# Performance work log

Measured on AMD Instinct MI355X. Metric: run time of the kernel, lower is better.

Reference implementation:

```python
import jax, jax.numpy as jnp
import numpy as np

V, BLOCK, L, H, C = 50257, 1024, 4, 12, 768
HS = C // H  # 64
EPS = 1e-6  # flax LayerNorm default


def _ln(x, scale, bias):
    mu = jnp.mean(x, axis=-1, keepdims=True)
    var = jnp.var(x, axis=-1, keepdims=True)
    return (x - mu) * jax.lax.rsqrt(var + EPS) * scale + bias


def setup_inputs() -> dict:
    key = jax.random.key(0)
    ks = jax.random.split(key, 12)
    B, T = 2, 1024
    inp = {
        'idx': jax.random.randint(ks[0], (B, T), 0, V),
        'targets': jax.random.randint(ks[1], (B, T), 0, V),
        'wte': jax.random.normal(ks[2], (V, C), jnp.float32) * 0.02,
        'wpe': jax.random.normal(ks[3], (BLOCK, C), jnp.float32) * 0.02,
        'ln1_s': jnp.ones((L, C), jnp.float32),
        'ln1_b': jnp.zeros((L, C), jnp.float32),
        'attn_k': jax.random.normal(ks[4], (L, C, H, 3 * HS), jnp.float32) * 0.02,
        'attn_b': jnp.zeros((L, H, 3 * HS), jnp.float32),
        'aproj_k': jax.random.normal(ks[5], (L, C, C), jnp.float32) * 0.02,
        'aproj_b': jnp.zeros((L, C), jnp.float32),
        'ln2_s': jnp.ones((L, C), jnp.float32),
        'ln2_b': jnp.zeros((L, C), jnp.float32),
        'fc_k': jax.random.normal(ks[6], (L, C, 4 * C), jnp.float32) * 0.02,
        'fc_b': jnp.zeros((L, 4 * C), jnp.float32),
        'mproj_k': jax.random.normal(ks[7], (L, 4 * C, C), jnp.float32) * 0.02,
        'mproj_b': jnp.zeros((L, C), jnp.float32),
        'lnf_s': jnp.ones((C,), jnp.float32),
        'lnf_b': jnp.zeros((C,), jnp.float32),
    }
    return inp


def _block(x, ln1_s, ln1_b, Wqkv, bqkv, Wo, bo, ln2_s, ln2_b, Wfc, bfc, Wmp, bmp, mask):
    B, T, _ = x.shape
    h = _ln(x, ln1_s, ln1_b)
    qkv = jnp.einsum('btc,chd->bhtd', h, Wqkv) + bqkv[:, None, :]  # [B,H,T,3HS]
    q, k, v = jnp.split(qkv, 3, axis=-1)
    att = jnp.einsum('bhtd,bhsd->bhts', q, k) * (1.0 / jnp.sqrt(jnp.float32(HS)))
    att = jnp.where(mask, att, -jnp.inf)
    att = jax.nn.softmax(att, axis=-1)
    y = jnp.einsum('bhts,bhsd->bthd', att, v).reshape(B, T, C)
    x = x + y @ Wo + bo
    h = _ln(x, ln2_s, ln2_b)
    h = jax.nn.gelu(h @ Wfc + bfc, approximate=True)
    x = x + h @ Wmp + bmp
    return x


def reference(idx, targets, wte, wpe, ln1_s, ln1_b, attn_k, attn_b, aproj_k, aproj_b,
              ln2_s, ln2_b, fc_k, fc_b, mproj_k, mproj_b, lnf_s, lnf_b):
    B, T = idx.shape
    x = wte[idx] + wpe[jnp.arange(T)][None]  # [B,T,C]
    mask = jnp.tril(jnp.ones((T, T), bool))[None, None]
    for l in range(L):
        x = _block(x, ln1_s[l], ln1_b[l], attn_k[l], attn_b[l], aproj_k[l], aproj_b[l],
                   ln2_s[l], ln2_b[l], fc_k[l], fc_b[l], mproj_k[l], mproj_b[l], mask)
    x = _ln(x, lnf_s, lnf_b)
    logits = jnp.einsum('btc,vc->btv', x, wte)  # tied output projection (wte.attend)
    logp = jax.nn.log_softmax(logits, axis=-1)
    loss = -jnp.mean(jnp.take_along_axis(logp, targets[..., None], axis=-1))
    return logits, loss
```

## Files before the change

### kernel.cpp

```cpp
#include <hip/hip_runtime.h>
#include <hip/hip_bf16.h>
#include <math.h>

typedef __attribute__((ext_vector_type(8))) short bf16x8;
typedef __attribute__((ext_vector_type(4))) float f32x4;

static constexpr int Bv   = 2;
static constexpr int Tv   = 1024;
static constexpr int Cv   = 768;
static constexpr int Hv   = 12;
static constexpr int Lv   = 4;
static constexpr int Vv   = 50257;
static constexpr int Mv   = 2048;
static constexpr int NTv  = 393;
static constexpr float EPSv = 1e-6f;

__device__ __forceinline__ void gload16(const void* g, void* l) {
    __builtin_amdgcn_global_load_lds((const __attribute__((address_space(1))) void*)g,
                                     (__attribute__((address_space(3))) void*)l, 16, 0, 0);
}
template<int N>
__device__ __forceinline__ void waitvm_barrier() {
    if constexpr (N == 0)      asm volatile("s_waitcnt vmcnt(0)\ns_barrier" ::: "memory");
    else if constexpr (N == 2) asm volatile("s_waitcnt vmcnt(2)\ns_barrier" ::: "memory");
    else if constexpr (N == 3) asm volatile("s_waitcnt vmcnt(3)\ns_barrier" ::: "memory");
    else if constexpr (N == 4) asm volatile("s_waitcnt vmcnt(4)\ns_barrier" ::: "memory");
    else if constexpr (N == 6) asm volatile("s_waitcnt vmcnt(6)\ns_barrier" ::: "memory");
    else                       asm volatile("s_waitcnt vmcnt(8)\ns_barrier" ::: "memory");
}
__device__ __forceinline__ void lgkm0_barrier() {
    asm volatile("s_waitcnt lgkmcnt(0)\ns_barrier" ::: "memory");
}

__global__ void embed_kernel(const int* __restrict__ idx,
                             const float* __restrict__ wte,
                             const float* __restrict__ wpe,
                             float* __restrict__ x) {
    int row = blockIdx.x;
    int t   = row & (Tv - 1);
    int tok = idx[row];
    const float* src = wte + (size_t)tok * Cv;
    const float* pos = wpe + (size_t)t * Cv;
    float* dst = x + (size_t)row * Cv;
    for (int c = threadIdx.x; c < Cv; c += 256)
        dst[c] = src[c] + pos[c];
}

__device__ __forceinline__ ushort4 pack4bf(float4 v) {
    ushort4 u;
    u.x = __bfloat16_as_ushort(__float2bfloat16(v.x));
    u.y = __bfloat16_as_ushort(__float2bfloat16(v.y));
    u.z = __bfloat16_as_ushort(__float2bfloat16(v.z));
    u.w = __bfloat16_as_ushort(__float2bfloat16(v.w));
    return u;
}

__global__ void ln_kernel(const float* __restrict__ in,
                          const float* __restrict__ sc,
                          const float* __restrict__ bi,
                          __hip_bfloat16* __restrict__ out) {
    int row  = blockIdx.x * 4 + (threadIdx.x >> 6);
    int lane = threadIdx.x & 63;
    const float4* xr = (const float4*)(in + (size_t)row * Cv);
    float4 a = xr[lane], b = xr[lane + 64], c = xr[lane + 128];
    float sum = a.x + a.y + a.z + a.w + b.x + b.y + b.z + b.w + c.x + c.y + c.z + c.w;
    float sq  = a.x*a.x + a.y*a.y + a.z*a.z + a.w*a.w
              + b.x*b.x + b.y*b.y + b.z*b.z + b.w*b.w
              + c.x*c.x + c.y*c.y + c.z*c.z + c.w*c.w;
    #pragma unroll
    for (int off = 32; off; off >>= 1) {
        sum += __shfl_xor(sum, off, 64);
        sq  += __shfl_xor(sq,  off, 64);
    }
    float mean = sum * (1.0f / Cv);
    float var  = sq * (1.0f / Cv) - mean * mean;
    float rs   = rsqrtf(var + EPSv);
    const float4* s4 = (const float4*)sc;
    const float4* b4 = (const float4*)bi;
    ushort4* orow = (ushort4*)(out + (size_t)row * Cv);
    #pragma unroll
    for (int i = 0; i < 3; ++i) {
        float4 v = (i == 0) ? a : (i == 1) ? b : c;
        float4 s = s4[lane + 64 * i];
        float4 t = b4[lane + 64 * i];
        float4 o;
        o.x = (v.x - mean) * rs * s.x + t.x;
        o.y = (v.y - mean) * rs * s.y + t.y;
        o.z = (v.z - mean) * rs * s.z + t.z;
        o.w = (v.w - mean) * rs * s.w + t.w;
        orow[lane + 64 * i] = pack4bf(o);
    }
}

__global__ void wtrans_kernel(const float* __restrict__ in,
                              __hip_bfloat16* __restrict__ out, int K, int N) {
    __shared__ float tile[32][33];
    int k0 = blockIdx.y * 32, n0 = blockIdx.x * 32;
    int tx = threadIdx.x & 31, ty = threadIdx.x >> 5;
    #pragma unroll
    for (int i = 0; i < 4; ++i)
        tile[ty + i * 8][tx] = in[(size_t)(k0 + ty + i * 8) * N + n0 + tx];
    __syncthreads();
    #pragma unroll
    for (int i = 0; i < 4; ++i)
        out[(size_t)(n0 + ty + i * 8) * K + k0 + tx] =
            __float2bfloat16(tile[tx][ty + i * 8]);
}

__global__ void cvt_kernel(const float* __restrict__ in,
                           __hip_bfloat16* __restrict__ out, int n4) {
    int stride = gridDim.x * 256;
    for (int i = blockIdx.x * 256 + threadIdx.x; i < n4; i += stride) {
        float4 v = ((const float4*)in)[i];
        ((ushort4*)out)[i] = pack4bf(v);
    }
}

__global__ void vtrans_kernel(const __hip_bfloat16* __restrict__ qkv,
                              __hip_bfloat16* __restrict__ vt) {
    __shared__ __hip_bfloat16 tile[32][33];
    int bh = blockIdx.z;
    int b = bh / Hv, h = bh % Hv;
    int t0 = blockIdx.x * 32, d0 = blockIdx.y * 32;
    int tx = threadIdx.x & 31, ty = threadIdx.x >> 5;
    #pragma unroll
    for (int i = 0; i < 4; ++i)
        tile[ty + i * 8][tx] =
            qkv[(size_t)(b * Tv + t0 + ty + i * 8) * 2304 + h * 192 + 128 + d0 + tx];
    __syncthreads();
    #pragma unroll
    for (int i = 0; i < 4; ++i)
        vt[((size_t)bh * 64 + d0 + ty + i * 8) * Tv + t0 + tx] = tile[tx][ty + i * 8];
}

template<int EPI, int BM>
__launch_bounds__(256)
__global__ void gemm_bf16(const __hip_bfloat16* __restrict__ A,
                          const __hip_bfloat16* __restrict__ Bt,
                          const float* __restrict__ bias,
                          const float* R, float* Cf,
                          __hip_bfloat16* __restrict__ Cb,
                          int M, int N, int K) {
    constexpr int FM  = BM / 32;
    constexpr int NA  = BM / 64;
    constexpr int LPT = NA + 1;
    __shared__ __hip_bfloat16 As[3][BM * 32];
    __shared__ __hip_bfloat16 Bs[3][64 * 32];
    int tid = threadIdx.x;
    int wave = tid >> 6, lane = tid & 63;
    int wr = wave >> 1, wc = wave & 1;
    int rowBase = blockIdx.y * BM, colBase = blockIdx.x * 64;

    f32x4 acc[FM][2] = {};

    int srow  = wave * 16 + (lane >> 2);
    int skcol = (lane & 3) * 8;
    const __hip_bfloat16* Ap0 = A + (size_t)(rowBase + srow) * K + skcol;
    const __hip_bfloat16* Ap1 = (NA > 1) ? (Ap0 + (size_t)64 * K) : Ap0;
    const __hip_bfloat16* Bp0 = Bt + (size_t)(colBase + srow) * K + skcol;
    int ldso = wave * 512;

    int aoff = (wr * (BM / 2) + (lane & 15)) * 32 + (lane >> 4) * 8;
    int boff = (wc * 32 + (lane & 15)) * 32 + (lane >> 4) * 8;

    auto stage = [&](int buf) {
        gload16(Ap0, &As[buf][ldso]);
        if constexpr (NA > 1) gload16(Ap1, &As[buf][2048 + ldso]);
        gload16(Bp0, &Bs[buf][ldso]);
        Ap0 += 32;
        if constexpr (NA > 1) Ap1 += 32;
        Bp0 += 32;
    };

    stage(0); stage(1); stage(2);

    int nt = K / 32;
    int cur = 0;
    for (int t = 0; t < nt; ++t) {
        if (t < nt - 2)       waitvm_barrier<2 * LPT>();
        else if (t == nt - 2) waitvm_barrier<LPT>();
        else                  waitvm_barrier<0>();

        bf16x8 av[FM], bv[2];
        #pragma unroll
        for (int m = 0; m < FM; ++m) av[m] = *(const bf16x8*)&As[cur][aoff + m * 512];
        #pragma unroll
        for (int n = 0; n < 2; ++n)  bv[n] = *(const bf16x8*)&Bs[cur][boff + n * 512];
        lgkm0_barrier();

        if (t + 3 < nt) stage(cur);

        #pragma unroll
        for (int m = 0; m < FM; ++m)
            #pragma unroll
            for (int n = 0; n < 2; ++n)
                acc[m][n] = __builtin_amdgcn_mfma_f32_16x16x32_bf16(
                    av[m], bv[n], acc[m][n], 0, 0, 0);
        cur = (cur == 2) ? 0 : cur + 1;
    }

    int fq = lane >> 4, fr = lane & 15;
    #pragma unroll
    for (int m = 0; m < FM; ++m) {
        #pragma unroll
        for (int n = 0; n < 2; ++n) {
            f32x4 v = acc[m][n];
            int col = colBase + wc * 32 + n * 16 + fr;
            #pragma unroll
            for (int j = 0; j < 4; ++j) {
                int row = rowBase + wr * (BM / 2) + m * 16 + fq * 4 + j;
                float val = v[j] + bias[col];
                if (EPI == 1) {
                    val += R[(size_t)row * N + col];
                    Cf[(size_t)row * N + col] = val;
                } else {
                    if (EPI == 2) {
                        float u = val;
                        float cc = 0.7978845608028654f * (u + 0.044715f * u * u * u);
                        val = 0.5f * u * (1.0f + tanhf(cc));
                    }
                    Cb[(size_t)row * N + col] = __float2bfloat16(val);
                }
            }
        }
    }
}

__launch_bounds__(256)
__global__ void attn_kernel(const __hip_bfloat16* __restrict__ qkv,
                            const __hip_bfloat16* __restrict__ vt,
                            __hip_bfloat16* __restrict__ att) {
    __shared__ __hip_bfloat16 Qs[64 * 64];
    __shared__ __hip_bfloat16 Ks[64 * 64];
    __shared__ __hip_bfloat16 Vs[64 * 64];
    __shared__ __hip_bfloat16 Ps[64 * 64];
    int bh = blockIdx.x;
    int b = bh / Hv, h = bh % Hv;
    int qt = (int)gridDim.y - 1 - (int)blockIdx.y;
    int q0 = qt * 64;
    int tid = threadIdx.x, wave = tid >> 6, lane = tid & 63;
    int g = lane >> 4, fr = lane & 15;
    int srow8 = lane >> 3, sc8 = lane & 7;

    const __hip_bfloat16* qbase = qkv + (size_t)(b * Tv + q0) * 2304 + h * 192;
    #pragma unroll
    for (int i = 0; i < 2; ++i) {
        int row = wave * 16 + i * 8 + srow8;
        gload16(qbase + (size_t)row * 2304 + ((sc8 ^ (row & 7)) * 8),
                Qs + (wave * 16 + i * 8) * 64);
    }

    f32x4 accO[4] = {};
    float mrun[4] = {-1e30f, -1e30f, -1e30f, -1e30f};
    float lrun[4] = {0.f, 0.f, 0.f, 0.f};

    for (int kv = 0; kv <= qt; ++kv) {
        int s0 = kv * 64;
        __syncthreads();
        const __hip_bfloat16* kbase = qkv + (size_t)(b * Tv + s0) * 2304 + h * 192 + 64;
        const __hip_bfloat16* vbase = vt + (size_t)bh * 64 * Tv + s0;
        #pragma unroll
        for (int i = 0; i < 2; ++i) {
            int row = wave * 16 + i * 8 + srow8;
            gload16(kbase + (size_t)row * 2304 + ((sc8 ^ (row & 7)) * 8),
                    Ks + (wave * 16 + i * 8) * 64);
            gload16(vbase + (size_t)row * Tv + ((sc8 ^ (row & 7)) * 8),
                    Vs + (wave * 16 + i * 8) * 64);
        }
        __syncthreads();

        f32x4 s4[4] = {};
        #pragma unroll
        for (int kk = 0; kk < 2; ++kk) {
            int qrow = wave * 16 + fr;
            bf16x8 qa = *(const bf16x8*)&Qs[qrow * 64 + (((g + 4 * kk) ^ (fr & 7)) * 8)];
            #pragma unroll
            for (int n = 0; n < 4; ++n) {
                int krow = n * 16 + fr;
                bf16x8 kb = *(const bf16x8*)&Ks[krow * 64 + (((g + 4 * kk) ^ (fr & 7)) * 8)];
                s4[n] = __builtin_amdgcn_mfma_f32_16x16x32_bf16(qa, kb, s4[n], 0, 0, 0);
            }
        }

        bool dia = (kv == qt);
        #pragma unroll
        for (int j = 0; j < 4; ++j) {
            int qg = q0 + wave * 16 + g * 4 + j;
            float sj[4], mx = -1e30f;
            #pragma unroll
            for (int n = 0; n < 4; ++n) {
                float v = s4[n][j] * 0.125f;
                if (dia && (s0 + n * 16 + fr) > qg) v = -1e30f;
                sj[n] = v;
                mx = fmaxf(mx, v);
            }
            #pragma unroll
            for (int off = 1; off < 16; off <<= 1)
                mx = fmaxf(mx, __shfl_xor(mx, off, 64));
            float mnew = fmaxf(mrun[j], mx);
            float ps = 0.f;
            unsigned short pb[4];
            #pragma unroll
            for (int n = 0; n < 4; ++n) {
                float p = __expf(sj[n] - mnew);
                __hip_bfloat16 pc = __float2bfloat16(p);
                pb[n] = __bfloat16_as_ushort(pc);
                ps += __bfloat162float(pc);
            }
            #pragma unroll
            for (int off = 1; off < 16; off <<= 1)
                ps += __shfl_xor(ps, off, 64);
            float cr = __expf(mrun[j] - mnew);
            lrun[j] = lrun[j] * cr + ps;
            mrun[j] = mnew;
            int prow = wave * 16 + g * 4 + j;
            #pragma unroll
            for (int n = 0; n < 4; ++n) {
                int byteoff = (32 * n + 2 * fr) ^ ((prow & 7) << 4);
                ((unsigned short*)Ps)[prow * 64 + (byteoff >> 1)] = pb[n];
            }
            #pragma unroll
            for (int n = 0; n < 4; ++n) accO[n][j] *= cr;
        }
        __syncthreads();

        #pragma unroll
        for (int kk = 0; kk < 2; ++kk) {
            int prow = wave * 16 + fr;
            bf16x8 pa = *(const bf16x8*)&Ps[prow * 64 + (((g + 4 * kk) ^ (fr & 7)) * 8)];
            #pragma unroll
            for (int n = 0; n < 4; ++n) {
                int vrow = n * 16 + fr;
                bf16x8 vb = *(const bf16x8*)&Vs[vrow * 64 + (((g + 4 * kk) ^ (fr & 7)) * 8)];
                accO[n] = __builtin_amdgcn_mfma_f32_16x16x32_bf16(pa, vb, accO[n], 0, 0, 0);
            }
        }
    }

    #pragma unroll
    for (int j = 0; j < 4; ++j) {
        float inv = 1.0f / lrun[j];
        int row = b * Tv + q0 + wave * 16 + g * 4 + j;
        #pragma unroll
        for (int n = 0; n < 4; ++n)
            att[(size_t)row * Cv + h * 64 + n * 16 + fr] =
                __float2bfloat16(accO[n][j] * inv);
    }
}

__launch_bounds__(256)
__global__ void lmhead_kernel(const __hip_bfloat16* __restrict__ A,
                              const __hip_bfloat16* __restrict__ Bt,
                              float* __restrict__ Cf,
                              float* __restrict__ pLse) {
    constexpr int K = Cv, N = Vv;
    __shared__ __hip_bfloat16 As[3][4096];
    __shared__ __hip_bfloat16 Bs[3][4096];
    __shared__ float ps2[2][128];

    int bid = blockIdx.x;
    int nid = (bid & 7) * (NTv * 16 / 8) + (bid >> 3);
    int rowT = nid & 15, colT = nid >> 4;
    int rowBase = rowT * 128, colBase = colT * 128;

    int tid = threadIdx.x, wave = tid >> 6, lane = tid & 63;
    int wr = wave >> 1, wc = wave & 1;

    f32x4 acc[4][4] = {};

    int srow  = wave * 16 + (lane >> 2);
    int skcol = (lane & 3) * 8;
    const __hip_bfloat16* Ap  = A + (size_t)(rowBase + srow) * K + skcol;
    const __hip_bfloat16* Ap2 = Ap + (size_t)64 * K;
    int brow1 = colBase + srow;
    int brow2 = brow1 + 64;
    const __hip_bfloat16* Bp  = Bt + (size_t)brow1 * K + skcol;
    const __hip_bfloat16* Bp2 = Bt + (size_t)(brow2 < N ? brow2 : N - 1) * K + skcol;
    int ldso = wave * 512;

    int aoff = (wr * 64 + (lane & 15)) * 32 + (lane >> 4) * 8;
    int boff = (wc * 64 + (lane & 15)) * 32 + (lane >> 4) * 8;

    auto stage = [&](int buf) {
        gload16(Ap,  &As[buf][ldso]);
        gload16(Ap2, &As[buf][2048 + ldso]);
        gload16(Bp,  &Bs[buf][ldso]);
        gload16(Bp2, &Bs[buf][2048 + ldso]);
        Ap += 32; Ap2 += 32; Bp += 32; Bp2 += 32;
    };

    stage(0); stage(1); stage(2);

    constexpr int nt = K / 32;
    int cur = 0;
    for (int t = 0; t < nt; ++t) {
        if (t < nt - 2)       waitvm_barrier<8>();
        else if (t == nt - 2) waitvm_barrier<4>();
        else                  waitvm_barrier<0>();

        bf16x8 av[4], bv[4];
        #pragma unroll
        for (int m = 0; m < 4; ++m) av[m] = *(const bf16x8*)&As[cur][aoff + m * 512];
        #pragma unroll
        for (int n = 0; n < 4; ++n) bv[n] = *(const bf16x8*)&Bs[cur][boff + n * 512];
        lgkm0_barrier();

        if (t + 3 < nt) stage(cur);

        #pragma unroll
        for (int m = 0; m < 4; ++m)
            #pragma unroll
            for (int n = 0; n < 4; ++n)
                acc[m][n] = __builtin_amdgcn_mfma_f32_16x16x32_bf16(
                    av[m], bv[n], acc[m][n], 0, 0, 0);
        cur = (cur == 2) ? 0 : cur + 1;
    }

    int fq = lane >> 4, fr = lane & 15;

    #pragma unroll
    for (int m = 0; m < 4; ++m) {
        #pragma unroll
        for (int j = 0; j < 4; ++j) {
            int row = rowBase + wr * 64 + m * 16 + fq * 4 + j;
            float s = 0.f;
            #pragma unroll
            for (int n = 0; n < 4; ++n) {
                int col = colBase + wc * 64 + n * 16 + fr;
                float v = acc[m][n][j];
                if (col < N) {
                    Cf[(size_t)row * N + col] = v;
                    s += __expf(v);
                }
            }
            #pragma unroll
            for (int off = 1; off < 16; off <<= 1)
                s += __shfl_xor(s, off, 64);
            if (fr == 0)
                ps2[wc][wr * 64 + m * 16 + fq * 4 + j] = s;
        }
    }
    __syncthreads();
    if (tid < 128)
        pLse[(size_t)(rowBase + tid) * NTv + colT] = ps2[0][tid] + ps2[1][tid];
}

__global__ void plse_reduce_kernel(const float* __restrict__ pLse,
                                   const float* __restrict__ logits,
                                   const int* __restrict__ targets,
                                   float* __restrict__ rloss) {
    int row  = blockIdx.x * 4 + (threadIdx.x >> 6);
    int lane = threadIdx.x & 63;
    const float* pr = pLse + (size_t)row * NTv;
    float l = 0.f;
    for (int i = lane; i < NTv; i += 64) l += pr[i];
    #pragma unroll
    for (int off = 32; off; off >>= 1) l += __shfl_xor(l, off, 64);
    if (lane == 0)
        rloss[row] = logf(l) - logits[(size_t)row * Vv + targets[row]];
}

__global__ void loss_final_kernel(const float* __restrict__ rloss,
                                  float* __restrict__ out, int out_size) {
    float s = 0.f;
    for (int i = threadIdx.x; i < Mv; i += 256) s += rloss[i];
    #pragma unroll
    for (int off = 32; off; off >>= 1) s += __shfl_xor(s, off, 64);
    __shared__ float sw[4];
    int wave = threadIdx.x >> 6, lane = threadIdx.x & 63;
    if (lane == 0) sw[wave] = s;
    __syncthreads();
    if (threadIdx.x == 0)
        out[out_size - 1] = (sw[0] + sw[1] + sw[2] + sw[3]) / (float)Mv;
}

extern "C" void kernel_launch(void* const* d_in, const int* in_sizes, int n_in,
                              void* d_out, int out_size, void* d_ws, size_t ws_size,
                              hipStream_t stream) {
    const int*   idx     = (const int*)  d_in[0];
    const int*   targets = (const int*)  d_in[1];
    const float* wte     = (const float*)d_in[2];
    const float* wpe     = (const float*)d_in[3];
    const float* ln1_s   = (const float*)d_in[4];
    const float* ln1_b   = (const float*)d_in[5];
    const float* attn_k  = (const float*)d_in[6];
    const float* attn_b  = (const float*)d_in[7];
    const float* aproj_k = (const float*)d_in[8];
    const float* aproj_b = (const float*)d_in[9];
    const float* ln2_s   = (const float*)d_in[10];
    const float* ln2_b   = (const float*)d_in[11];
    const float* fc_k    = (const float*)d_in[12];
    const float* fc_b    = (const float*)d_in[13];
    const float* mproj_k = (const float*)d_in[14];
    const float* mproj_b = (const float*)d_in[15];
    const float* lnf_s   = (const float*)d_in[16];
    const float* lnf_b   = (const float*)d_in[17];

    float* out = (float*)d_out;
    char* ws  = (char*)d_ws;
    char* ob  = (char*)d_out;

    constexpr size_t NEED = 83568128ULL;
    if (ws_size < NEED) return;

    __hip_bfloat16* wte_bf = (__hip_bfloat16*)(ws + 0);
    __hip_bfloat16* h_bf   = (__hip_bfloat16*)(ws + 77194752);
    float*          pLse   = (float*)(ws + 80340480);
    float*          rloss  = (float*)(ws + 83559936);

    float*          x      = (float*)(ob + 0);
    __hip_bfloat16* qkv_bf = (__hip_bfloat16*)(ob + 6291456);
    __hip_bfloat16* vt_bf  = (__hip_bfloat16*)(ob + 15728640);
    __hip_bfloat16* att_bf = (__hip_bfloat16*)(ob + 18874368);
    __hip_bfloat16* fco_bf = (__hip_bfloat16*)(ob + 22020096);
    __hip_bfloat16* w0     = (__hip_bfloat16*)(ob + 34603008);
    __hip_bfloat16* w1     = (__hip_bfloat16*)(ob + 38141952);
    __hip_bfloat16* w2     = (__hip_bfloat16*)(ob + 39321600);
    __hip_bfloat16* w3     = (__hip_bfloat16*)(ob + 44040192);

    embed_kernel<<<Mv, 256, 0, stream>>>(idx, wte, wpe, x);

    for (int l = 0; l < Lv; ++l) {
        wtrans_kernel<<<dim3(72, 24), 256, 0, stream>>>(
            attn_k + (size_t)l * Cv * 2304, w0, Cv, 2304);
        wtrans_kernel<<<dim3(24, 24), 256, 0, stream>>>(
            aproj_k + (size_t)l * Cv * Cv, w1, Cv, Cv);
        wtrans_kernel<<<dim3(96, 24), 256, 0, stream>>>(
            fc_k + (size_t)l * Cv * 3072, w2, Cv, 3072);
        wtrans_kernel<<<dim3(24, 96), 256, 0, stream>>>(
            mproj_k + (size_t)l * 3072 * Cv, w3, 3072, Cv);

        ln_kernel<<<512, 256, 0, stream>>>(x, ln1_s + l * Cv, ln1_b + l * Cv, h_bf);
        gemm_bf16<0, 128><<<dim3(36, 16), 256, 0, stream>>>(
            h_bf, w0, attn_b + l * 2304, nullptr, nullptr, qkv_bf, Mv, 2304, Cv);
        vtrans_kernel<<<dim3(32, 2, 24), 256, 0, stream>>>(qkv_bf, vt_bf);
        attn_kernel<<<dim3(24, 16), 256, 0, stream>>>(qkv_bf, vt_bf, att_bf);
        gemm_bf16<1, 64><<<dim3(12, 32), 256, 0, stream>>>(
            att_bf, w1, aproj_b + l * Cv, x, x, nullptr, Mv, Cv, Cv);
        ln_kernel<<<512, 256, 0, stream>>>(x, ln2_s + l * Cv, ln2_b + l * Cv, h_bf);
        gemm_bf16<2, 128><<<dim3(48, 16), 256, 0, stream>>>(
            h_bf, w2, fc_b + l * 3072, nullptr, nullptr, fco_bf, Mv, 3072, Cv);
        gemm_bf16<1, 64><<<dim3(12, 32), 256, 0, stream>>>(
            fco_bf, w3, mproj_b + l * Cv, x, x, nullptr, Mv, Cv, 3072);
    }

    ln_kernel<<<512, 256, 0, stream>>>(x, lnf_s, lnf_b, h_bf);
    cvt_kernel<<<2048, 256, 0, stream>>>(wte, wte_bf, (Vv * Cv) / 4);
    lmhead_kernel<<<16 * NTv, 256, 0, stream>>>(h_bf, wte_bf, out, pLse);
    plse_reduce_kernel<<<512, 256, 0, stream>>>(pLse, out, targets, rloss);
    loss_final_kernel<<<1, 256, 0, stream>>>(rloss, out, out_size);
}
```

Before: 986.8 us.

## Enlarge LM-head tiles to 256x256 with swizzled LDS and batch weight transposes

The LM-head GEMM now uses 256x256 output tiles with 512 threads, a 64-wide K step with double buffering, and an XOR-swizzled LDS layout. Wave priority is raised around the MFMA bursts. This cuts global/L2 traffic per FLOP and halves the partial-LSE columns. The per-layer weight transposes are collapsed into four launches that cover all layers, storing each layer's transposed weights separately. The larger tile means higher register pressure, only one block per CU, and more waste in the last partial vocabulary tile.

```diff
diff --git a/kernel.cpp b/kernel.cpp
--- a/kernel.cpp
+++ b/kernel.cpp
@@ -12,7 +12,7 @@
 static constexpr int Lv   = 4;
 static constexpr int Vv   = 50257;
 static constexpr int Mv   = 2048;
-static constexpr int NTv  = 393;
+static constexpr int NT2  = 197;
 static constexpr float EPSv = 1e-6f;
 
 __device__ __forceinline__ void gload16(const void* g, void* l) {
@@ -93,8 +93,11 @@
 }
 
 __global__ void wtrans_kernel(const float* __restrict__ in,
-                              __hip_bfloat16* __restrict__ out, int K, int N) {
+                              __hip_bfloat16* __restrict__ out, int K, int N,
+                              size_t inLS, size_t outLS) {
     __shared__ float tile[32][33];
+    in  += (size_t)blockIdx.z * inLS;
+    out += (size_t)blockIdx.z * outLS;
     int k0 = blockIdx.y * 32, n0 = blockIdx.x * 32;
     int tx = threadIdx.x & 31, ty = threadIdx.x >> 5;
     #pragma unroll
@@ -348,81 +351,107 @@
     }
 }
 
-__launch_bounds__(256)
+__launch_bounds__(512, 1)
 __global__ void lmhead_kernel(const __hip_bfloat16* __restrict__ A,
                               const __hip_bfloat16* __restrict__ Bt,
                               float* __restrict__ Cf,
                               float* __restrict__ pLse) {
     constexpr int K = Cv, N = Vv;
-    __shared__ __hip_bfloat16 As[3][4096];
-    __shared__ __hip_bfloat16 Bs[3][4096];
-    __shared__ float ps2[2][128];
+    constexpr int nt = K / 64;
+    __shared__ __hip_bfloat16 As[2][16384];
+    __shared__ __hip_bfloat16 Bs[2][16384];
+    __shared__ float ps[4][256];
 
     int bid = blockIdx.x;
-    int nid = (bid & 7) * (NTv * 16 / 8) + (bid >> 3);
-    int rowT = nid & 15, colT = nid >> 4;
-    int rowBase = rowT * 128, colBase = colT * 128;
-
-    int tid = threadIdx.x, wave = tid >> 6, lane = tid & 63;
-    int wr = wave >> 1, wc = wave & 1;
-
-    f32x4 acc[4][4] = {};
-
-    int srow  = wave * 16 + (lane >> 2);
-    int skcol = (lane & 3) * 8;
-    const __hip_bfloat16* Ap  = A + (size_t)(rowBase + srow) * K + skcol;
-    const __hip_bfloat16* Ap2 = Ap + (size_t)64 * K;
-    int brow1 = colBase + srow;
-    int brow2 = brow1 + 64;
-    const __hip_bfloat16* Bp  = Bt + (size_t)brow1 * K + skcol;
-    const __hip_bfloat16* Bp2 = Bt + (size_t)(brow2 < N ? brow2 : N - 1) * K + skcol;
-    int ldso = wave * 512;
-
-    int aoff = (wr * 64 + (lane & 15)) * 32 + (lane >> 4) * 8;
-    int boff = (wc * 64 + (lane & 15)) * 32 + (lane >> 4) * 8;
-
-    auto stage = [&](int buf) {
-        gload16(Ap,  &As[buf][ldso]);
-        gload16(Ap2, &As[buf][2048 + ldso]);
-        gload16(Bp,  &Bs[buf][ldso]);
-        gload16(Bp2, &Bs[buf][2048 + ldso]);
-        Ap += 32; Ap2 += 32; Bp += 32; Bp2 += 32;
+    int nid = (bid & 7) * NT2 + (bid >> 3);
+    int rowT = nid & 7, colT = nid >> 3;
+    int rowBase = rowT * 256, colBase = colT * 256;
+
+    int tid = threadIdx.x;
+    int wv = tid >> 6, lane = tid & 63;
+    int wr = wv >> 2, wc = wv & 3;
+    int fq = lane >> 4, fr = lane & 15;
+    int fr7 = fr & 7;
+
+    f32x4 acc[8][4] = {};
+
+    int r8 = lane >> 3;
+    int cOff = ((lane & 7) ^ r8) * 8;
+    const __hip_bfloat16* ApS[4];
+    const __hip_bfloat16* BpS[4];
+    #pragma unroll
+    for (int i = 0; i < 4; ++i) {
+        int rit = wv * 32 + i * 8 + r8;
+        ApS[i] = A + (size_t)(rowBase + rit) * K + cOff;
+        int rb = colBase + rit;
+        if (rb >= N) rb = N - 1;
+        BpS[i] = Bt + (size_t)rb * K + cOff;
+    }
+
+    auto stage = [&](int buf, int tile) {
+        int k0 = tile * 64;
+        #pragma unroll
+        for (int i = 0; i < 4; ++i)
+            gload16(ApS[i] + k0, &As[buf][(wv * 4 + i) * 512]);
+        #pragma unroll
+        for (int i = 0; i < 4; ++i)
+            gload16(BpS[i] + k0, &Bs[buf][(wv * 4 + i) * 512]);
     };
 
-    stage(0); stage(1); stage(2);
-
-    constexpr int nt = K / 32;
-    int cur = 0;
+    stage(0, 0);
+    stage(1, 1);
+    waitvm_barrier<8>();
+
     for (int t = 0; t < nt; ++t) {
-        if (t < nt - 2)       waitvm_barrier<8>();
-        else if (t == nt - 2) waitvm_barrier<4>();
-        else                  waitvm_barrier<0>();
-
-        bf16x8 av[4], bv[4];
-        #pragma unroll
-        for (int m = 0; m < 4; ++m) av[m] = *(const bf16x8*)&As[cur][aoff + m * 512];
-        #pragma unroll
-        for (int n = 0; n < 4; ++n) bv[n] = *(const bf16x8*)&Bs[cur][boff + n * 512];
-        lgkm0_barrier();
-
-        if (t + 3 < nt) stage(cur);
-
-        #pragma unroll
-        for (int m = 0; m < 4; ++m)
+        int cur = t & 1;
+        const __hip_bfloat16* Ab = &As[cur][0];
+        const __hip_bfloat16* Bb = &Bs[cur][0];
+
+        bf16x8 av0[8], bv0[4];
+        #pragma unroll
+        for (int m = 0; m < 8; ++m)
+            av0[m] = *(const bf16x8*)&Ab[(wr * 128 + m * 16 + fr) * 64 + ((fq ^ fr7) * 8)];
+        #pragma unroll
+        for (int n = 0; n < 4; ++n)
+            bv0[n] = *(const bf16x8*)&Bb[(wc * 64 + n * 16 + fr) * 64 + ((fq ^ fr7) * 8)];
+        __builtin_amdgcn_s_setprio(1);
+        #pragma unroll
+        for (int m = 0; m < 8; ++m)
             #pragma unroll
             for (int n = 0; n < 4; ++n)
                 acc[m][n] = __builtin_amdgcn_mfma_f32_16x16x32_bf16(
-                    av[m], bv[n], acc[m][n], 0, 0, 0);
-        cur = (cur == 2) ? 0 : cur + 1;
-    }
-
-    int fq = lane >> 4, fr = lane & 15;
-
-    #pragma unroll
-    for (int m = 0; m < 4; ++m) {
+                    av0[m], bv0[n], acc[m][n], 0, 0, 0);
+        __builtin_amdgcn_s_setprio(0);
+
+        bf16x8 av1[8], bv1[4];
+        #pragma unroll
+        for (int m = 0; m < 8; ++m)
+            av1[m] = *(const bf16x8*)&Ab[(wr * 128 + m * 16 + fr) * 64 + (((4 + fq) ^ fr7) * 8)];
+        #pragma unroll
+        for (int n = 0; n < 4; ++n)
+            bv1[n] = *(const bf16x8*)&Bb[(wc * 64 + n * 16 + fr) * 64 + (((4 + fq) ^ fr7) * 8)];
+        lgkm0_barrier();
+
+        if (t + 2 < nt) stage(cur, t + 2);
+
+        __builtin_amdgcn_s_setprio(1);
+        #pragma unroll
+        for (int m = 0; m < 8; ++m)
+            #pragma unroll
+            for (int n = 0; n < 4; ++n)
+                acc[m][n] = __builtin_amdgcn_mfma_f32_16x16x32_bf16(
+                    av1[m], bv1[n], acc[m][n], 0, 0, 0);
+        __builtin_amdgcn_s_setprio(0);
+
+        if (t + 2 < nt) waitvm_barrier<8>();
+        else            waitvm_barrier<0>();
+    }
+
+    #pragma unroll
+    for (int m = 0; m < 8; ++m) {
         #pragma unroll
         for (int j = 0; j < 4; ++j) {
-            int row = rowBase + wr * 64 + m * 16 + fq * 4 + j;
+            int row = rowBase + wr * 128 + m * 16 + fq * 4 + j;
             float s = 0.f;
             #pragma unroll
             for (int n = 0; n < 4; ++n) {
@@ -437,12 +466,13 @@
             for (int off = 1; off < 16; off <<= 1)
                 s += __shfl_xor(s, off, 64);
             if (fr == 0)
-                ps2[wc][wr * 64 + m * 16 + fq * 4 + j] = s;
+                ps[wc][wr * 128 + m * 16 + fq * 4 + j] = s;
         }
     }
     __syncthreads();
-    if (tid < 128)
-        pLse[(size_t)(rowBase + tid) * NTv + colT] = ps2[0][tid] + ps2[1][tid];
+    if (tid < 256)
+        pLse[(size_t)(rowBase + tid) * NT2 + colT] =
+            ps[0][tid] + ps[1][tid] + ps[2][tid] + ps[3][tid];
 }
 
 __global__ void plse_reduce_kernel(const float* __restrict__ pLse,
@@ -451,9 +481,9 @@
                                    float* __restrict__ rloss) {
     int row  = blockIdx.x * 4 + (threadIdx.x >> 6);
     int lane = threadIdx.x & 63;
-    const float* pr = pLse + (size_t)row * NTv;
+    const float* pr = pLse + (size_t)row * NT2;
     float l = 0.f;
-    for (int i = lane; i < NTv; i += 64) l += pr[i];
+    for (int i = lane; i < NT2; i += 64) l += pr[i];
     #pragma unroll
     for (int off = 32; off; off >>= 1) l += __shfl_xor(l, off, 64);
     if (lane == 0)
@@ -500,13 +530,13 @@
     char* ws  = (char*)d_ws;
     char* ob  = (char*)d_out;
 
-    constexpr size_t NEED = 83568128ULL;
+    constexpr size_t NEED = 81962496ULL;
     if (ws_size < NEED) return;
 
     __hip_bfloat16* wte_bf = (__hip_bfloat16*)(ws + 0);
     __hip_bfloat16* h_bf   = (__hip_bfloat16*)(ws + 77194752);
     float*          pLse   = (float*)(ws + 80340480);
-    float*          rloss  = (float*)(ws + 83559936);
+    float*          rloss  = (float*)(ws + 81954304);
 
     float*          x      = (float*)(ob + 0);
     __hip_bfloat16* qkv_bf = (__hip_bfloat16*)(ob + 6291456);
@@ -514,39 +544,43 @@
     __hip_bfloat16* att_bf = (__hip_bfloat16*)(ob + 18874368);
     __hip_bfloat16* fco_bf = (__hip_bfloat16*)(ob + 22020096);
     __hip_bfloat16* w0     = (__hip_bfloat16*)(ob + 34603008);
-    __hip_bfloat16* w1     = (__hip_bfloat16*)(ob + 38141952);
-    __hip_bfloat16* w2     = (__hip_bfloat16*)(ob + 39321600);
-    __hip_bfloat16* w3     = (__hip_bfloat16*)(ob + 44040192);
+    __hip_bfloat16* w1     = (__hip_bfloat16*)(ob + 48758784);
+    __hip_bfloat16* w2     = (__hip_bfloat16*)(ob + 53477376);
+    __hip_bfloat16* w3     = (__hip_bfloat16*)(ob + 72351744);
 
     embed_kernel<<<Mv, 256, 0, stream>>>(idx, wte, wpe, x);
 
+    wtrans_kernel<<<dim3(72, 24, 4), 256, 0, stream>>>(
+        attn_k, w0, Cv, 2304, (size_t)Cv * 2304, (size_t)2304 * Cv);
+    wtrans_kernel<<<dim3(24, 24, 4), 256, 0, stream>>>(
+        aproj_k, w1, Cv, Cv, (size_t)Cv * Cv, (size_t)Cv * Cv);
+    wtrans_kernel<<<dim3(96, 24, 4), 256, 0, stream>>>(
+        fc_k, w2, Cv, 3072, (size_t)Cv * 3072, (size_t)3072 * Cv);
+    wtrans_kernel<<<dim3(24, 96, 4), 256, 0, stream>>>(
+        mproj_k, w3, 3072, Cv, (size_t)3072 * Cv, (size_t)Cv * 3072);
+
     for (int l = 0; l < Lv; ++l) {
-        wtrans_kernel<<<dim3(72, 24), 256, 0, stream>>>(
-            attn_k + (size_t)l * Cv * 2304, w0, Cv, 2304);
-        wtrans_kernel<<<dim3(24, 24), 256, 0, stream>>>(
-            aproj_k + (size_t)l * Cv * Cv, w1, Cv, Cv);
-        wtrans_kernel<<<dim3(96, 24), 256, 0, stream>>>(
-            fc_k + (size_t)l * Cv * 3072, w2, Cv, 3072);
-        wtrans_kernel<<<dim3(24, 96), 256, 0, stream>>>(
-            mproj_k + (size_t)l * 3072 * Cv, w3, 3072, Cv);
-
         ln_kernel<<<512, 256, 0, stream>>>(x, ln1_s + l * Cv, ln1_b + l * Cv, h_bf);
         gemm_bf16<0, 128><<<dim3(36, 16), 256, 0, stream>>>(
-            h_bf, w0, attn_b + l * 2304, nullptr, nullptr, qkv_bf, Mv, 2304, Cv);
+            h_bf, w0 + (size_t)l * 2304 * Cv, attn_b + l * 2304, nullptr, nullptr,
+            qkv_bf, Mv, 2304, Cv);
         vtrans_kernel<<<dim3(32, 2, 24), 256, 0, stream>>>(qkv_bf, vt_bf);
         attn_kernel<<<dim3(24, 16), 256, 0, stream>>>(qkv_bf, vt_bf, att_bf);
         gemm_bf16<1, 64><<<dim3(12, 32), 256, 0, stream>>>(
-            att_bf, w1, aproj_b + l * Cv, x, x, nullptr, Mv, Cv, Cv);
+            att_bf, w1 + (size_t)l * Cv * Cv, aproj_b + l * Cv, x, x, nullptr,
+            Mv, Cv, Cv);
         ln_kernel<<<512, 256, 0, stream>>>(x, ln2_s + l * Cv, ln2_b + l * Cv, h_bf);
         gemm_bf16<2, 128><<<dim3(48, 16), 256, 0, stream>>>(
-            h_bf, w2, fc_b + l * 3072, nullptr, nullptr, fco_bf, Mv, 3072, Cv);
+            h_bf, w2 + (size_t)l * 3072 * Cv, fc_b + l * 3072, nullptr, nullptr,
+            fco_bf, Mv, 3072, Cv);
         gemm_bf16<1, 64><<<dim3(12, 32), 256, 0, stream>>>(
-            fco_bf, w3, mproj_b + l * Cv, x, x, nullptr, Mv, Cv, 3072);
+            fco_bf, w3 + (size_t)l * Cv * 3072, mproj_b + l * Cv, x, x, nullptr,
+            Mv, Cv, 3072);
     }
 
     ln_kernel<<<512, 256, 0, stream>>>(x, lnf_s, lnf_b, h_bf);
     cvt_kernel<<<2048, 256, 0, stream>>>(wte, wte_bf, (Vv * Cv) / 4);
-    lmhead_kernel<<<16 * NTv, 256, 0, stream>>>(h_bf, wte_bf, out, pLse);
+    lmhead_kernel<<<8 * NT2, 512, 0, stream>>>(h_bf, wte_bf, out, pLse);
     plse_reduce_kernel<<<512, 256, 0, stream>>>(pLse, out, targets, rloss);
     loss_final_kernel<<<1, 256, 0, stream>>>(rloss, out, out_size);
 }
```

New measurement: 942.1 us. -4.5%, faster.
